# Performance work log

Hardware: AMD Instinct MI355X
Metric: run time of the kernel (lower is better)

The kernel has to match this reference:

```python
import jax, jax.numpy as jnp
import numpy as np

D_MODEL = 1024
NUM_HEADS = 16
D_K = D_MODEL // NUM_HEADS
NEG = -1000000000.0


def setup_inputs() -> dict:
    key = jax.random.key(0)
    ks = jax.random.split(key, 5)
    B, S = 1, 4096
    x = jax.random.normal(ks[0], (B, S, D_MODEL), dtype=jnp.float32)
    # torch nn.Linear weights are [out_features, in_features]; scale like kaiming-uniform-ish
    std = 1.0 / np.sqrt(D_MODEL)
    W_q = jax.random.normal(ks[1], (D_MODEL, D_MODEL), dtype=jnp.float32) * std
    W_k = jax.random.normal(ks[2], (D_MODEL, D_MODEL), dtype=jnp.float32) * std
    W_v = jax.random.normal(ks[3], (D_MODEL, D_MODEL), dtype=jnp.float32) * std
    W_o = jax.random.normal(ks[4], (D_MODEL, D_MODEL), dtype=jnp.float32) * std
    return {"x": x, "W_q": W_q, "W_k": W_k, "W_v": W_v, "W_o": W_o}


def reference(x, W_q, W_k, W_v, W_o):
    B, S, _ = x.shape
    scale = jnp.asarray(np.sqrt(D_K), dtype=x.dtype)
    # Linear: y = x @ W.T  (torch convention, weight [out, in])
    def proj(W):
        y = jnp.einsum('bsd,ed->bse', x, W)
        return y.reshape(B, S, NUM_HEADS, D_K).transpose(0, 2, 1, 3)  # [B,H,S,Dk]
    Q, K, V = proj(W_q), proj(W_k), proj(W_v)
    scores = jnp.einsum('bhqd,bhkd->bhqk', Q, K) / scale  # [B,H,S,S]
    causal = jnp.triu(jnp.ones((S, S), dtype=bool), k=1)  # True above diagonal
    scores = jnp.where(causal[None, None], jnp.asarray(NEG, x.dtype), scores)
    attn = jax.nn.softmax(scores, axis=-1)
    # dropout p=0.0 -> identity
    ctx = jnp.einsum('bhqk,bhkd->bhqd', attn, V)
    ctx = ctx.transpose(0, 2, 1, 3).reshape(B, S, D_MODEL)
    return jnp.einsum('bsd,ed->bse', ctx, W_o)
```

## Files before the change

### kernel.cpp

```cpp
#include <hip/hip_runtime.h>
#include <stdint.h>

#define S_LEN 4096
#define DM 1024
#define NH 16
#define DKH 64
#define LDQ (3 * DM)

typedef __attribute__((ext_vector_type(8))) __bf16 bf16x8;
typedef __attribute__((ext_vector_type(8))) short s16x8;
typedef __attribute__((ext_vector_type(4))) float f32x4;

__device__ inline unsigned short f2bf(float f) {
  unsigned int u = __builtin_bit_cast(unsigned int, f);
  u += 0x7fff + ((u >> 16) & 1);
  return (unsigned short)(u >> 16);
}
__device__ inline float bf2f(unsigned short u) {
  return __builtin_bit_cast(float, (unsigned int)u << 16);
}

__device__ inline f32x4 mfma16(s16x8 a, s16x8 b, f32x4 c) {
  return __builtin_amdgcn_mfma_f32_16x16x32_bf16(
      __builtin_bit_cast(bf16x8, a), __builtin_bit_cast(bf16x8, b), c, 0, 0, 0);
}

__device__ inline void gld_lds16(const unsigned short* g, unsigned short* l) {
  __builtin_amdgcn_global_load_lds(
      (const __attribute__((address_space(1))) unsigned int*)g,
      (__attribute__((address_space(3))) unsigned int*)l, 16, 0, 0);
}

__global__ void convert_f32_bf16(const float* __restrict__ in,
                                 unsigned short* __restrict__ out, int n4) {
  int i = blockIdx.x * blockDim.x + threadIdx.x;
  if (i >= n4) return;
  float4 v = reinterpret_cast<const float4*>(in)[i];
  ushort4 o;
  o.x = f2bf(v.x); o.y = f2bf(v.y); o.z = f2bf(v.z); o.w = f2bf(v.w);
  reinterpret_cast<ushort4*>(out)[i] = o;
}

__device__ inline void storeC(unsigned short* C, size_t i, float v) { C[i] = f2bf(v); }
__device__ inline void storeC(float* C, size_t i, float v) { C[i] = v; }

template <typename OutT>
__global__ __launch_bounds__(256) void gemm_bt(const unsigned short* __restrict__ A,
                                               const unsigned short* __restrict__ B,
                                               OutT* __restrict__ C, int M, int N, int K) {
  __shared__ __align__(16) unsigned short lds_a[128 * 64];
  __shared__ __align__(16) unsigned short lds_b[128 * 64];
  const int tid = threadIdx.x;
  const int lane = tid & 63;
  const int w = tid >> 6;
  const int wr = w >> 1, wc = w & 1;
  const int l15 = lane & 15, lhi = lane >> 4;
  const int bm0 = blockIdx.x * 128, bn0 = blockIdx.y * 128;
  const int srow = lane >> 3;
  const int scol = (lane & 7) * 8;

  f32x4 acc[4][4] = {};

  for (int k0 = 0; k0 < K; k0 += 64) {
    __syncthreads();
#pragma unroll
    for (int i = 0; i < 4; ++i) {
      const int base = i * 2048 + w * 512;
      const int row = i * 32 + w * 8 + srow;
      gld_lds16(A + (size_t)(bm0 + row) * K + k0 + scol, lds_a + base);
      gld_lds16(B + (size_t)(bn0 + row) * K + k0 + scol, lds_b + base);
    }
    __syncthreads();
#pragma unroll
    for (int kk = 0; kk < 2; ++kk) {
      s16x8 af[4], bfr[4];
#pragma unroll
      for (int mi = 0; mi < 4; ++mi)
        af[mi] = *(const s16x8*)&lds_a[(wr * 64 + mi * 16 + l15) * 64 + kk * 32 + lhi * 8];
#pragma unroll
      for (int ni = 0; ni < 4; ++ni)
        bfr[ni] = *(const s16x8*)&lds_b[(wc * 64 + ni * 16 + l15) * 64 + kk * 32 + lhi * 8];
#pragma unroll
      for (int mi = 0; mi < 4; ++mi)
#pragma unroll
        for (int ni = 0; ni < 4; ++ni)
          acc[mi][ni] = mfma16(af[mi], bfr[ni], acc[mi][ni]);
    }
  }
#pragma unroll
  for (int mi = 0; mi < 4; ++mi)
#pragma unroll
    for (int ni = 0; ni < 4; ++ni)
#pragma unroll
      for (int r = 0; r < 4; ++r) {
        int row = bm0 + wr * 64 + mi * 16 + lhi * 4 + r;
        int col = bn0 + wc * 64 + ni * 16 + l15;
        storeC(C, (size_t)row * N + col, acc[mi][ni][r]);
      }
}

__global__ __launch_bounds__(256) void transpose_v(const unsigned short* __restrict__ QKV,
                                                   unsigned short* __restrict__ vTg) {
  const int s0 = blockIdx.x * 64;
  const int h = blockIdx.y;
  __shared__ __align__(16) unsigned short t[64][72];
  const int r = threadIdx.x >> 2;
  const int c = (threadIdx.x & 3) * 16;
  const unsigned short* src = QKV + (size_t)(s0 + r) * LDQ + 2 * DM + h * DKH + c;
#pragma unroll
  for (int j = 0; j < 16; j += 4)
    *(ushort4*)&t[r][c + j] = *(const ushort4*)(src + j);
  __syncthreads();
  const int d = threadIdx.x >> 2;
  const int sc = (threadIdx.x & 3) * 16;
  unsigned short* dst = vTg + (size_t)(h * DKH + d) * S_LEN + s0 + sc;
#pragma unroll
  for (int j = 0; j < 16; j += 4) {
    ushort4 v;
    v.x = t[sc + j + 0][d]; v.y = t[sc + j + 1][d];
    v.z = t[sc + j + 2][d]; v.w = t[sc + j + 3][d];
    *(ushort4*)(dst + j) = v;
  }
}

__device__ inline void stage_kv(const unsigned short* __restrict__ Kp,
                                const unsigned short* __restrict__ vTg,
                                unsigned short* lk, unsigned short* lv,
                                int kb, int h, int tid) {
  const int w = tid >> 6, l = tid & 63;
  const int sub = l >> 3;
  const int src_col = 8 * ((l & 7) ^ sub);
#pragma unroll
  for (int i = 0; i < 2; ++i) {
    const int row = i * 32 + w * 8 + sub;
    gld_lds16(Kp + (size_t)(kb + row) * LDQ + h * DKH + src_col,
              lk + (i * 32 + w * 8) * 64);
    gld_lds16(vTg + (size_t)(h * DKH + row) * S_LEN + kb + src_col,
              lv + (i * 32 + w * 8) * 64);
  }
}

template <bool MASK>
__device__ inline void attn_tile_lds(const unsigned short* __restrict__ lk,
                                     const unsigned short* __restrict__ lv,
                                     unsigned short (*pb)[72], const s16x8 qf[2],
                                     int kb, int qrow0, int l15, int lhi,
                                     f32x4 o[4], float m_r[4], float l_r[4]) {
  const int sw = (l15 & 7) * 8;
  f32x4 sf[4];
#pragma unroll
  for (int st = 0; st < 4; ++st) {
    f32x4 acc = {};
#pragma unroll
    for (int kk = 0; kk < 2; ++kk) {
      s16x8 kf = *(const s16x8*)&lk[(st * 16 + l15) * 64 + ((kk * 32 + lhi * 8) ^ sw)];
      acc = mfma16(qf[kk], kf, acc);
    }
    sf[st] = acc;
  }
  if (MASK) {
#pragma unroll
    for (int st = 0; st < 4; ++st) {
      const int key = kb + st * 16 + l15;
#pragma unroll
      for (int r = 0; r < 4; ++r) {
        const int qrow = qrow0 + lhi * 4 + r;
        if (key > qrow) sf[st][r] = -1e30f;
      }
    }
  }
  float alpha[4];
#pragma unroll
  for (int r = 0; r < 4; ++r) {
    float mx = fmaxf(fmaxf(sf[0][r], sf[1][r]), fmaxf(sf[2][r], sf[3][r]));
#pragma unroll
    for (int d = 1; d < 16; d <<= 1) mx = fmaxf(mx, __shfl_xor(mx, d));
    const float mn = fmaxf(m_r[r], mx);
    alpha[r] = __expf(m_r[r] - mn);
    m_r[r] = mn;
    float rs = 0.f;
#pragma unroll
    for (int st = 0; st < 4; ++st) {
      const float p = __expf(sf[st][r] - mn);
      sf[st][r] = p;
      rs += p;
    }
#pragma unroll
    for (int d = 1; d < 16; d <<= 1) rs += __shfl_xor(rs, d);
    l_r[r] = l_r[r] * alpha[r] + rs;
  }
#pragma unroll
  for (int st = 0; st < 4; ++st)
#pragma unroll
    for (int r = 0; r < 4; ++r)
      pb[lhi * 4 + r][st * 16 + l15] = f2bf(sf[st][r]);
#pragma unroll
  for (int n = 0; n < 4; ++n)
#pragma unroll
    for (int r = 0; r < 4; ++r) o[n][r] *= alpha[r];
#pragma unroll
  for (int kk = 0; kk < 2; ++kk) {
    s16x8 pa = *(const s16x8*)&pb[l15][kk * 32 + lhi * 8];
#pragma unroll
    for (int n = 0; n < 4; ++n) {
      s16x8 vb = *(const s16x8*)&lv[(n * 16 + l15) * 64 + ((kk * 32 + lhi * 8) ^ sw)];
      o[n] = mfma16(pa, vb, o[n]);
    }
  }
}

__global__ __launch_bounds__(256) void attn_causal3(const unsigned short* __restrict__ QKV,
                                                    const unsigned short* __restrict__ vTg,
                                                    unsigned short* __restrict__ CTX) {
  const int flat = blockIdx.x + 32 * blockIdx.y;
  const int swz = (flat & 7) * 64 + (flat >> 3);
  const int pr = swz & 31;
  const int h = swz >> 5;
  const int tid = threadIdx.x;
  const int lane = tid & 63, w = tid >> 6;
  const int l15 = lane & 15, lhi = lane >> 4;

  __shared__ __align__(16) unsigned short lk[2][64 * 64];
  __shared__ __align__(16) unsigned short lv[2][64 * 64];
  __shared__ __align__(16) unsigned short pbuf[4][16][72];
  unsigned short (*pb)[72] = pbuf[w];

  const unsigned short* Qp = QKV;
  const unsigned short* Kp = QKV + DM;

#pragma unroll 1
  for (int half = 0; half < 2; ++half) {
    const int qt = half ? (63 - pr) : pr;
    const int qrow0 = qt * 64 + w * 16;
    s16x8 qf[2];
#pragma unroll
    for (int kk = 0; kk < 2; ++kk) {
      s16x8 q = *(const s16x8*)&Qp[(size_t)(qrow0 + l15) * LDQ + h * DKH + kk * 32 + lhi * 8];
#pragma unroll
      for (int e = 0; e < 8; ++e)
        q[e] = (short)f2bf(bf2f((unsigned short)q[e]) * 0.125f);
      qf[kk] = q;
    }
    f32x4 o[4] = {};
    float m_r[4], l_r[4];
#pragma unroll
    for (int r = 0; r < 4; ++r) { m_r[r] = -1e30f; l_r[r] = 0.f; }

    __syncthreads();
    stage_kv(Kp, vTg, lk[0], lv[0], 0, h, tid);
    int cur = 0;
#pragma unroll 1
    for (int kbi = 0; kbi <= qt; ++kbi) {
      __syncthreads();
      if (kbi < qt)
        stage_kv(Kp, vTg, lk[cur ^ 1], lv[cur ^ 1], (kbi + 1) * 64, h, tid);
      if (kbi < qt)
        attn_tile_lds<false>(lk[cur], lv[cur], pb, qf, kbi * 64, qrow0, l15, lhi, o, m_r, l_r);
      else
        attn_tile_lds<true>(lk[cur], lv[cur], pb, qf, kbi * 64, qrow0, l15, lhi, o, m_r, l_r);
      cur ^= 1;
    }

#pragma unroll
    for (int n = 0; n < 4; ++n)
#pragma unroll
      for (int r = 0; r < 4; ++r) {
        const int qrow = qrow0 + lhi * 4 + r;
        CTX[(size_t)qrow * DM + h * DKH + n * 16 + l15] = f2bf(o[n][r] / l_r[r]);
      }
  }
}

extern "C" void kernel_launch(void* const* d_in, const int* in_sizes, int n_in,
                              void* d_out, int out_size, void* d_ws, size_t ws_size,
                              hipStream_t stream) {
  const float* x  = (const float*)d_in[0];
  const float* Wq = (const float*)d_in[1];
  const float* Wk = (const float*)d_in[2];
  const float* Wv = (const float*)d_in[3];
  const float* Wo = (const float*)d_in[4];
  float* out = (float*)d_out;
  char* ws = (char*)d_ws;

  unsigned short* x_bf  = (unsigned short*)(ws + 0);
  unsigned short* wqkv  = (unsigned short*)(ws + (size_t)8 * 1024 * 1024);
  unsigned short* wo_bf = (unsigned short*)(ws + (size_t)14 * 1024 * 1024);
  unsigned short* qkv   = (unsigned short*)(ws + (size_t)16 * 1024 * 1024);
  unsigned short* ctx   = (unsigned short*)(ws + (size_t)40 * 1024 * 1024);
  unsigned short* vTg   = (unsigned short*)(ws + (size_t)48 * 1024 * 1024);

  const int n4x = S_LEN * DM / 4;
  convert_f32_bf16<<<(n4x + 255) / 256, 256, 0, stream>>>(x, x_bf, n4x);
  const int w4 = DM * DM / 4;
  convert_f32_bf16<<<(w4 + 255) / 256, 256, 0, stream>>>(Wq, wqkv, w4);
  convert_f32_bf16<<<(w4 + 255) / 256, 256, 0, stream>>>(Wk, wqkv + DM * DM, w4);
  convert_f32_bf16<<<(w4 + 255) / 256, 256, 0, stream>>>(Wv, wqkv + 2 * DM * DM, w4);
  convert_f32_bf16<<<(w4 + 255) / 256, 256, 0, stream>>>(Wo, wo_bf, w4);

  dim3 g1(S_LEN / 128, (3 * DM) / 128);
  gemm_bt<unsigned short><<<g1, 256, 0, stream>>>(x_bf, wqkv, qkv, S_LEN, 3 * DM, DM);

  dim3 gt(S_LEN / 64, NH);
  transpose_v<<<gt, 256, 0, stream>>>(qkv, vTg);

  dim3 g2(32, NH);
  attn_causal3<<<g2, 256, 0, stream>>>(qkv, vTg, ctx);

  dim3 g3(S_LEN / 128, DM / 128);
  gemm_bt<float><<<g3, 256, 0, stream>>>(ctx, wo_bf, out, S_LEN, DM, DM);
}
```

Baseline: 297.7 us.

## Split causal attention into one q-tile per block with XCD-aware mapping and lazy rescale

The attention kernel now launches 1024 blocks, one 64-row query tile each, instead of 512 blocks that each processed a balanced pair of tiles. Tiles are assigned so that each XCD holds two heads, with light and heavy tiles interleaved. The online softmax skips rescaling the running output and sum unless some row's max grows by more than 8, which cuts exp and multiply work. The P buffer loses its padding and uses an XOR swizzle for conflict-free LDS access, and bf16 conversion now uses the hardware intrinsic. Risks are load imbalance from tiles of very different cost, and precision limits from the lazy-rescale threshold.

```diff
diff --git a/kernel.cpp b/kernel.cpp
--- a/kernel.cpp
+++ b/kernel.cpp
@@ -1,4 +1,5 @@
 #include <hip/hip_runtime.h>
+#include <hip/hip_bf16.h>
 #include <stdint.h>
 
 #define S_LEN 4096
@@ -18,6 +19,9 @@
 }
 __device__ inline float bf2f(unsigned short u) {
   return __builtin_bit_cast(float, (unsigned int)u << 16);
+}
+__device__ inline unsigned short f2bf_hw(float f) {
+  return __builtin_bit_cast(unsigned short, __float2bfloat16(f));
 }
 
 __device__ inline f32x4 mfma16(s16x8 a, s16x8 b, f32x4 c) {
@@ -143,7 +147,7 @@
 template <bool MASK>
 __device__ inline void attn_tile_lds(const unsigned short* __restrict__ lk,
                                      const unsigned short* __restrict__ lv,
-                                     unsigned short (*pb)[72], const s16x8 qf[2],
+                                     unsigned short (*pb)[64], const s16x8 qf[2],
                                      int kb, int qrow0, int l15, int lhi,
                                      f32x4 o[4], float m_r[4], float l_r[4]) {
   const int sw = (l15 & 7) * 8;
@@ -169,38 +173,55 @@
       }
     }
   }
-  float alpha[4];
+  float mt[4];
 #pragma unroll
   for (int r = 0; r < 4; ++r) {
     float mx = fmaxf(fmaxf(sf[0][r], sf[1][r]), fmaxf(sf[2][r], sf[3][r]));
 #pragma unroll
     for (int d = 1; d < 16; d <<= 1) mx = fmaxf(mx, __shfl_xor(mx, d));
-    const float mn = fmaxf(m_r[r], mx);
-    alpha[r] = __expf(m_r[r] - mn);
-    m_r[r] = mn;
+    mt[r] = mx;
+  }
+  int grow = (mt[0] > m_r[0] + 8.f) | (mt[1] > m_r[1] + 8.f) |
+             (mt[2] > m_r[2] + 8.f) | (mt[3] > m_r[3] + 8.f);
+  const bool anyg = __any(grow);
+  float alpha[4];
+  if (anyg) {
+#pragma unroll
+    for (int r = 0; r < 4; ++r) {
+      const float mn = fmaxf(m_r[r], mt[r]);
+      alpha[r] = __expf(m_r[r] - mn);
+      m_r[r] = mn;
+    }
+  }
+#pragma unroll
+  for (int r = 0; r < 4; ++r) {
     float rs = 0.f;
 #pragma unroll
     for (int st = 0; st < 4; ++st) {
-      const float p = __expf(sf[st][r] - mn);
+      const float p = __expf(sf[st][r] - m_r[r]);
       sf[st][r] = p;
       rs += p;
     }
 #pragma unroll
     for (int d = 1; d < 16; d <<= 1) rs += __shfl_xor(rs, d);
-    l_r[r] = l_r[r] * alpha[r] + rs;
+    l_r[r] = (anyg ? l_r[r] * alpha[r] : l_r[r]) + rs;
+  }
+  if (anyg) {
+#pragma unroll
+    for (int n = 0; n < 4; ++n)
+#pragma unroll
+      for (int r = 0; r < 4; ++r) o[n][r] *= alpha[r];
   }
 #pragma unroll
   for (int st = 0; st < 4; ++st)
 #pragma unroll
-    for (int r = 0; r < 4; ++r)
-      pb[lhi * 4 + r][st * 16 + l15] = f2bf(sf[st][r]);
-#pragma unroll
-  for (int n = 0; n < 4; ++n)
-#pragma unroll
-    for (int r = 0; r < 4; ++r) o[n][r] *= alpha[r];
+    for (int r = 0; r < 4; ++r) {
+      const int row = lhi * 4 + r;
+      pb[row][(st * 16 + l15) ^ ((row & 7) * 8)] = f2bf_hw(sf[st][r]);
+    }
 #pragma unroll
   for (int kk = 0; kk < 2; ++kk) {
-    s16x8 pa = *(const s16x8*)&pb[l15][kk * 32 + lhi * 8];
+    s16x8 pa = *(const s16x8*)&pb[l15][(kk * 32 + lhi * 8) ^ sw];
 #pragma unroll
     for (int n = 0; n < 4; ++n) {
       s16x8 vb = *(const s16x8*)&lv[(n * 16 + l15) * 64 + ((kk * 32 + lhi * 8) ^ sw)];
@@ -209,66 +230,64 @@
   }
 }
 
-__global__ __launch_bounds__(256) void attn_causal3(const unsigned short* __restrict__ QKV,
+__global__ __launch_bounds__(256) void attn_causal4(const unsigned short* __restrict__ QKV,
                                                     const unsigned short* __restrict__ vTg,
                                                     unsigned short* __restrict__ CTX) {
-  const int flat = blockIdx.x + 32 * blockIdx.y;
-  const int swz = (flat & 7) * 64 + (flat >> 3);
-  const int pr = swz & 31;
-  const int h = swz >> 5;
+  const int flat = blockIdx.x + 64 * blockIdx.y;
+  const int xcd = flat & 7;
+  const int t = flat >> 3;
+  const int hb = t & 1;
+  const int j = t >> 1;
+  const int qt = (j & 1) ? (63 - (j >> 1)) : (j >> 1);
+  const int h = 2 * xcd + hb;
   const int tid = threadIdx.x;
   const int lane = tid & 63, w = tid >> 6;
   const int l15 = lane & 15, lhi = lane >> 4;
+  const int qrow0 = qt * 64 + w * 16;
 
   __shared__ __align__(16) unsigned short lk[2][64 * 64];
   __shared__ __align__(16) unsigned short lv[2][64 * 64];
-  __shared__ __align__(16) unsigned short pbuf[4][16][72];
-  unsigned short (*pb)[72] = pbuf[w];
+  __shared__ __align__(16) unsigned short pbuf[4][16][64];
+  unsigned short (*pb)[64] = pbuf[w];
 
   const unsigned short* Qp = QKV;
   const unsigned short* Kp = QKV + DM;
 
+  s16x8 qf[2];
+#pragma unroll
+  for (int kk = 0; kk < 2; ++kk) {
+    s16x8 q = *(const s16x8*)&Qp[(size_t)(qrow0 + l15) * LDQ + h * DKH + kk * 32 + lhi * 8];
+#pragma unroll
+    for (int e = 0; e < 8; ++e)
+      q[e] = (short)f2bf(bf2f((unsigned short)q[e]) * 0.125f);
+    qf[kk] = q;
+  }
+  f32x4 o[4] = {};
+  float m_r[4], l_r[4];
+#pragma unroll
+  for (int r = 0; r < 4; ++r) { m_r[r] = -1e30f; l_r[r] = 0.f; }
+
+  stage_kv(Kp, vTg, lk[0], lv[0], 0, h, tid);
+  int cur = 0;
 #pragma unroll 1
-  for (int half = 0; half < 2; ++half) {
-    const int qt = half ? (63 - pr) : pr;
-    const int qrow0 = qt * 64 + w * 16;
-    s16x8 qf[2];
-#pragma unroll
-    for (int kk = 0; kk < 2; ++kk) {
-      s16x8 q = *(const s16x8*)&Qp[(size_t)(qrow0 + l15) * LDQ + h * DKH + kk * 32 + lhi * 8];
-#pragma unroll
-      for (int e = 0; e < 8; ++e)
-        q[e] = (short)f2bf(bf2f((unsigned short)q[e]) * 0.125f);
-      qf[kk] = q;
-    }
-    f32x4 o[4] = {};
-    float m_r[4], l_r[4];
-#pragma unroll
-    for (int r = 0; r < 4; ++r) { m_r[r] = -1e30f; l_r[r] = 0.f; }
-
+  for (int kbi = 0; kbi <= qt; ++kbi) {
     __syncthreads();
-    stage_kv(Kp, vTg, lk[0], lv[0], 0, h, tid);
-    int cur = 0;
-#pragma unroll 1
-    for (int kbi = 0; kbi <= qt; ++kbi) {
-      __syncthreads();
-      if (kbi < qt)
-        stage_kv(Kp, vTg, lk[cur ^ 1], lv[cur ^ 1], (kbi + 1) * 64, h, tid);
-      if (kbi < qt)
-        attn_tile_lds<false>(lk[cur], lv[cur], pb, qf, kbi * 64, qrow0, l15, lhi, o, m_r, l_r);
-      else
-        attn_tile_lds<true>(lk[cur], lv[cur], pb, qf, kbi * 64, qrow0, l15, lhi, o, m_r, l_r);
-      cur ^= 1;
-    }
-
-#pragma unroll
-    for (int n = 0; n < 4; ++n)
-#pragma unroll
-      for (int r = 0; r < 4; ++r) {
-        const int qrow = qrow0 + lhi * 4 + r;
-        CTX[(size_t)qrow * DM + h * DKH + n * 16 + l15] = f2bf(o[n][r] / l_r[r]);
-      }
-  }
+    if (kbi < qt)
+      stage_kv(Kp, vTg, lk[cur ^ 1], lv[cur ^ 1], (kbi + 1) * 64, h, tid);
+    if (kbi < qt)
+      attn_tile_lds<false>(lk[cur], lv[cur], pb, qf, kbi * 64, qrow0, l15, lhi, o, m_r, l_r);
+    else
+      attn_tile_lds<true>(lk[cur], lv[cur], pb, qf, kbi * 64, qrow0, l15, lhi, o, m_r, l_r);
+    cur ^= 1;
+  }
+
+#pragma unroll
+  for (int n = 0; n < 4; ++n)
+#pragma unroll
+    for (int r = 0; r < 4; ++r) {
+      const int qrow = qrow0 + lhi * 4 + r;
+      CTX[(size_t)qrow * DM + h * DKH + n * 16 + l15] = f2bf_hw(o[n][r] / l_r[r]);
+    }
 }
 
 extern "C" void kernel_launch(void* const* d_in, const int* in_sizes, int n_in,
@@ -303,8 +322,8 @@
   dim3 gt(S_LEN / 64, NH);
   transpose_v<<<gt, 256, 0, stream>>>(qkv, vTg);
 
-  dim3 g2(32, NH);
-  attn_causal3<<<g2, 256, 0, stream>>>(qkv, vTg, ctx);
+  dim3 g2(64, NH);
+  attn_causal4<<<g2, 256, 0, stream>>>(qkv, vTg, ctx);
 
   dim3 g3(S_LEN / 128, DM / 128);
   gemm_bt<float><<<g3, 256, 0, stream>>>(ctx, wo_bf, out, S_LEN, DM, DM);
```

New measurement: 381.0 us. +28.0%, slower.
